# Kernel tuning notes

Measured on AMD Instinct MI355X. Metric: run time of the kernel, lower is better.

## Reference

```python
import jax, jax.numpy as jnp
import numpy as np
import math

S, B, E, H = 2048, 2, 1024, 16
D = E // H
LN_EPS = 1e-5


def setup_inputs() -> dict:
    key = jax.random.key(0)
    ks = jax.random.split(key, 8)
    src = jax.random.normal(ks[0], (S, B, E), dtype=jnp.float32)
    # causal attention mask: 1 = attend, 0 = masked
    src_mask = jnp.tril(jnp.ones((S, S), dtype=jnp.int32))
    in_proj_w = jax.random.normal(ks[1], (2 * E, E), dtype=jnp.float32) * 0.02
    in_proj_b = jnp.zeros((2 * E,), dtype=jnp.float32)
    out_proj_w = jax.random.normal(ks[2], (E, E), dtype=jnp.float32) * 0.02
    out_proj_b = jnp.zeros((E,), dtype=jnp.float32)
    ln_g = jnp.ones((E,), dtype=jnp.float32)
    ln_b = jnp.zeros((E,), dtype=jnp.float32)
    return {"src": src, "src_mask": src_mask, "in_proj_w": in_proj_w,
            "in_proj_b": in_proj_b, "out_proj_w": out_proj_w,
            "out_proj_b": out_proj_b, "ln_g": ln_g, "ln_b": ln_b}


def _layernorm(x, g, b):
    mu = jnp.mean(x, axis=-1, keepdims=True)
    var = jnp.mean(jnp.square(x - mu), axis=-1, keepdims=True)
    return (x - mu) * jax.lax.rsqrt(var + LN_EPS) * g + b


def reference(src, src_mask, in_proj_w, in_proj_b, out_proj_w, out_proj_b, ln_g, ln_b):
    # src: (S, B, E)
    x_norm = _layernorm(src, ln_g, ln_b)
    proj = jax.nn.silu(x_norm @ in_proj_w.T + in_proj_b)     # (S, B, 2E)
    qkv, u = jnp.split(proj, 2, axis=-1)                     # each (S, B, E)
    qkv = qkv.reshape(S, B, H, D)                            # q = k = v = qkv
    # scores: (B, H, S_q, S_k)
    scores = jnp.einsum('sbhd,tbhd->bhst', qkv, qkv) / math.sqrt(D)
    # torch does masked_fill(-inf) then silu; silu(-inf) -> 0 in the limit,
    # which is the intended semantics (masked positions contribute nothing).
    weights = jnp.where(src_mask[None, None, :, :] == 0, 0.0, jax.nn.silu(scores))
    # attn_dropout is identity at eval
    attn = jnp.einsum('bhst,tbhd->sbhd', weights, qkv).reshape(S, B, E)
    gated = attn * u
    out = src + (gated @ out_proj_w.T + out_proj_b)          # out_dropout = identity
    return out
```

## Files before the change

kernel.cpp:

```cpp
#include <hip/hip_runtime.h>


typedef __attribute__((ext_vector_type(8))) short  short8;
typedef __attribute__((ext_vector_type(4))) float  floatx4;
typedef __attribute__((ext_vector_type(4))) float  fvec4;
typedef __attribute__((ext_vector_type(4))) unsigned short usvec4;
typedef __attribute__((ext_vector_type(4))) int    intx4;

__device__ __forceinline__ unsigned short f2b(float f) {
  unsigned u = __builtin_bit_cast(unsigned, f);
  u += 0x7FFFu + ((u >> 16) & 1u);
  return (unsigned short)(u >> 16);
}
__device__ __forceinline__ unsigned short f2b_trunc(float f) {
  return (unsigned short)(__builtin_bit_cast(unsigned, f) >> 16);
}
__device__ __forceinline__ float b2f(unsigned short h) {
  unsigned u = ((unsigned)h) << 16;
  return __builtin_bit_cast(float, u);
}
__device__ __forceinline__ float silu_f(float x) {
  float e = __builtin_amdgcn_exp2f(-1.44269504f * x);
  return x * __builtin_amdgcn_rcpf(1.f + e);
}
__device__ __forceinline__ void async_copy16(void* lds, const void* g) {
  __builtin_amdgcn_global_load_lds(
      (__attribute__((address_space(1))) void*)(g),
      (__attribute__((address_space(3))) void*)(lds), 16, 0, 0);
}

__global__ void cvt_bf16(const float* __restrict__ s1, unsigned short* __restrict__ d1,
                         const float* __restrict__ s2, unsigned short* __restrict__ d2,
                         int n1, int ntot) {
  int i = blockIdx.x * 256 + threadIdx.x;
  if (i >= ntot) return;
  const float* s; unsigned short* d; int j;
  if (i < n1) { s = s1; d = d1; j = i; } else { s = s2; d = d2; j = i - n1; }
  fvec4 v = ((const fvec4*)s)[j];
  usvec4 o = { f2b(v.x), f2b(v.y), f2b(v.z), f2b(v.w) };
  ((usvec4*)d)[j] = o;
}

__global__ __launch_bounds__(256) void ln_kernel(
    const float* __restrict__ x, const float* __restrict__ g,
    const float* __restrict__ b, unsigned short* __restrict__ xn) {
  const int lane = threadIdx.x & 63;
  const int row = blockIdx.x * 4 + (threadIdx.x >> 6);
  const fvec4* xr = (const fvec4*)(x + (long)row * 1024);
  fvec4 v[4];
  float s = 0.f, s2 = 0.f;
  #pragma unroll
  for (int c = 0; c < 4; ++c) {
    v[c] = xr[lane + 64 * c];
    s  += v[c].x + v[c].y + v[c].z + v[c].w;
    s2 += v[c].x*v[c].x + v[c].y*v[c].y + v[c].z*v[c].z + v[c].w*v[c].w;
  }
  #pragma unroll
  for (int off = 32; off; off >>= 1) { s += __shfl_xor(s, off); s2 += __shfl_xor(s2, off); }
  float mu  = s * (1.f / 1024.f);
  float var = s2 * (1.f / 1024.f) - mu * mu;
  float rs  = rsqrtf(var + 1e-5f);
  usvec4* outr = (usvec4*)(xn + (long)row * 1024);
  #pragma unroll
  for (int c = 0; c < 4; ++c) {
    fvec4 gg = ((const fvec4*)g)[lane + 64 * c];
    fvec4 bb = ((const fvec4*)b)[lane + 64 * c];
    usvec4 o = { f2b((v[c].x - mu) * rs * gg.x + bb.x),
                 f2b((v[c].y - mu) * rs * gg.y + bb.y),
                 f2b((v[c].z - mu) * rs * gg.z + bb.z),
                 f2b((v[c].w - mu) * rs * gg.w + bb.w) };
    outr[lane + 64 * c] = o;
  }
}

__global__ __launch_bounds__(256, 2) void gemm_in(
    const unsigned short* __restrict__ A, const unsigned short* __restrict__ Bw,
    const float* __restrict__ bias,
    unsigned short* __restrict__ out0, unsigned short* __restrict__ out1) {
  __shared__ __align__(16) unsigned short sA[128 * 32];
  __shared__ __align__(16) unsigned short sB[128 * 32];
  const int t = threadIdx.x;
  const int lane = t & 63, l15 = lane & 15, quad = lane >> 4;
  const int w = t >> 6, wm = w >> 1, wn = w & 1;
  const int m0 = blockIdx.y * 128, n0 = blockIdx.x * 128;
  const int K = 1024;

  floatx4 acc[4][4];
  const floatx4 z4 = {0.f, 0.f, 0.f, 0.f};
  #pragma unroll
  for (int i = 0; i < 4; i++)
    #pragma unroll
    for (int j = 0; j < 4; j++) acc[i][j] = z4;

  for (int kt = 0; kt < 32; ++kt) {
    const int k0 = kt << 5;
    __syncthreads();
    #pragma unroll
    for (int c = 0; c < 2; ++c) {
      int slot = c * 256 + t;
      int row = slot >> 2, col = (slot & 3) << 3;
      async_copy16(&sA[slot * 8], &A[(m0 + row) * K + k0 + col]);
      async_copy16(&sB[slot * 8], &Bw[(n0 + row) * K + k0 + col]);
    }
    __syncthreads();
    short8 af[4], bf[4];
    #pragma unroll
    for (int mr = 0; mr < 4; mr++)
      af[mr] = *(const short8*)&sA[(wm * 64 + mr * 16 + l15) * 32 + quad * 8];
    #pragma unroll
    for (int nr = 0; nr < 4; nr++)
      bf[nr] = *(const short8*)&sB[(wn * 64 + nr * 16 + l15) * 32 + quad * 8];
    #pragma unroll
    for (int mr = 0; mr < 4; mr++)
      #pragma unroll
      for (int nr = 0; nr < 4; nr++)
        acc[mr][nr] = __builtin_amdgcn_mfma_f32_16x16x32_bf16(af[mr], bf[nr], acc[mr][nr], 0, 0, 0);
  }

  #pragma unroll
  for (int mr = 0; mr < 4; mr++) {
    int gm0 = m0 + wm * 64 + mr * 16 + quad * 4;
    #pragma unroll
    for (int nr = 0; nr < 4; nr++) {
      int gn = n0 + wn * 64 + nr * 16 + l15;
      float bv = bias[gn];
      unsigned short* dst = (gn < 1024) ? (out0 + gn) : (out1 + gn - 1024);
      #pragma unroll
      for (int r = 0; r < 4; r++) {
        float v = acc[mr][nr][r] + bv;
        dst[(long)(gm0 + r) * 1024] = f2b(silu_f(v));
      }
    }
  }
}

__global__ __launch_bounds__(256, 2) void gemm_out(
    const unsigned short* __restrict__ A, const unsigned short* __restrict__ Bw,
    const float* __restrict__ bias, const float* __restrict__ src,
    float* __restrict__ outf) {
  __shared__ __align__(16) unsigned short sA[128 * 32];
  __shared__ __align__(16) unsigned short sB[64 * 32];
  const int t = threadIdx.x;
  const int lane = t & 63, l15 = lane & 15, quad = lane >> 4;
  const int w = t >> 6;
  const int m0 = blockIdx.y * 128, n0 = blockIdx.x * 64;

  floatx4 acc[2][4];
  const floatx4 z4 = {0.f, 0.f, 0.f, 0.f};
  #pragma unroll
  for (int i = 0; i < 2; i++)
    #pragma unroll
    for (int j = 0; j < 4; j++) acc[i][j] = z4;

  for (int kt = 0; kt < 32; ++kt) {
    const int k0 = kt << 5;
    __syncthreads();
    #pragma unroll
    for (int c = 0; c < 2; ++c) {
      int slot = c * 256 + t;
      int row = slot >> 2, col = (slot & 3) << 3;
      async_copy16(&sA[slot * 8], &A[(m0 + row) * 1024 + k0 + col]);
    }
    { int row = t >> 2, col = (t & 3) << 3;
      async_copy16(&sB[t * 8], &Bw[(n0 + row) * 1024 + k0 + col]); }
    __syncthreads();
    short8 af[2], bf[4];
    #pragma unroll
    for (int mr = 0; mr < 2; mr++)
      af[mr] = *(const short8*)&sA[(w * 32 + mr * 16 + l15) * 32 + quad * 8];
    #pragma unroll
    for (int nr = 0; nr < 4; nr++)
      bf[nr] = *(const short8*)&sB[(nr * 16 + l15) * 32 + quad * 8];
    #pragma unroll
    for (int mr = 0; mr < 2; mr++)
      #pragma unroll
      for (int nr = 0; nr < 4; nr++)
        acc[mr][nr] = __builtin_amdgcn_mfma_f32_16x16x32_bf16(af[mr], bf[nr], acc[mr][nr], 0, 0, 0);
  }

  #pragma unroll
  for (int mr = 0; mr < 2; mr++) {
    int gm0 = m0 + w * 32 + mr * 16 + quad * 4;
    #pragma unroll
    for (int nr = 0; nr < 4; nr++) {
      int gn = n0 + nr * 16 + l15;
      float bv = bias[gn];
      #pragma unroll
      for (int r = 0; r < 4; r++) {
        long idx = (long)(gm0 + r) * 1024 + gn;
        outf[idx] = acc[mr][nr][r] + bv + src[idx];
      }
    }
  }
}

#define SKS 72
#define SVS 136
#define SPS 136
#define SOS 68
__global__ __launch_bounds__(256, 2) void attn_kernel(
    const unsigned short* __restrict__ qkv, const unsigned short* __restrict__ u,
    unsigned short* __restrict__ gated) {
  __shared__ __align__(16) unsigned char smem[128 * SKS * 2 + 64 * SVS * 2];
  unsigned short* sK  = (unsigned short*)smem;
  unsigned short* sP  = (unsigned short*)smem;
  unsigned short* sVt = (unsigned short*)(smem + 128 * SKS * 2);
  float*          sO  = (float*)smem;

  const int t = threadIdx.x, lane = t & 63, l15 = lane & 15, quad = lane >> 4;
  const int w = t >> 6;
  const int pair = blockIdx.x >> 5;
  const int bh = blockIdx.x & 31;
  const int b = bh >> 4, h = bh & 15;
  const long base = (long)b * 1024 + h * 64;
  const int rg = t >> 3, dg = t & 7;
  const int swz0 = (rg >> 1) + dg;
  const int d_rd = w * 16 + l15;
  const int rsw0 = quad + (d_rd & 7) + (d_rd >> 3);
  const floatx4 z4 = {0.f, 0.f, 0.f, 0.f};

  for (int half = 0; half < 2; ++half) {
    const int qi = half ? (31 - pair) : pair;
    const int q0 = qi * 64;
    const int nkt = (qi >> 1) + 1;

    if (half) __syncthreads();
    #pragma unroll
    for (int c = 0; c < 2; ++c) {
      int slot = c * 256 + t, row = slot >> 3, cg = slot & 7;
      *(short8*)&sK[row * SKS + cg * 8] =
          *(const short8*)&qkv[base + (long)(q0 + row) * 2048 + cg * 8];
    }
    __syncthreads();
    short8 qf[4][2];
    #pragma unroll
    for (int mr = 0; mr < 4; mr++)
      #pragma unroll
      for (int ks = 0; ks < 2; ks++)
        qf[mr][ks] = *(const short8*)&sK[(mr * 16 + l15) * SKS + ks * 32 + quad * 8];

    floatx4 oacc[4];
    #pragma unroll
    for (int i = 0; i < 4; i++) oacc[i] = z4;

    for (int kt = 0; kt < nkt; ++kt) {
      const int t0 = kt * 128;
      __syncthreads();
      short8 kv[4];
      #pragma unroll
      for (int i = 0; i < 4; ++i)
        kv[i] = *(const short8*)&qkv[base + (long)(t0 + rg * 4 + i) * 2048 + dg * 8];
      #pragma unroll
      for (int i = 0; i < 4; ++i)
        *(short8*)&sK[(rg * 4 + i) * SKS + dg * 8] = kv[i];
      {
        intx4 k0 = __builtin_bit_cast(intx4, kv[0]);
        intx4 k1 = __builtin_bit_cast(intx4, kv[1]);
        intx4 k2 = __builtin_bit_cast(intx4, kv[2]);
        intx4 k3 = __builtin_bit_cast(intx4, kv[3]);
        #pragma unroll
        for (int jj = 0; jj < 4; ++jj) {
          unsigned lo = __builtin_amdgcn_perm((unsigned)k1[jj], (unsigned)k0[jj], 0x05040100u);
          unsigned hi = __builtin_amdgcn_perm((unsigned)k3[jj], (unsigned)k2[jj], 0x05040100u);
          int j = 2 * jj, d = dg * 8 + j;
          int gsw = (swz0 + j) & 15;
          *(unsigned long long*)&sVt[d * SVS + gsw * 8 + (rg & 1) * 4] =
              (unsigned long long)lo | ((unsigned long long)hi << 32);
          lo = __builtin_amdgcn_perm((unsigned)k1[jj], (unsigned)k0[jj], 0x07060302u);
          hi = __builtin_amdgcn_perm((unsigned)k3[jj], (unsigned)k2[jj], 0x07060302u);
          j = 2 * jj + 1; d = dg * 8 + j;
          gsw = (swz0 + j) & 15;
          *(unsigned long long*)&sVt[d * SVS + gsw * 8 + (rg & 1) * 4] =
              (unsigned long long)lo | ((unsigned long long)hi << 32);
        }
      }
      __syncthreads();
      floatx4 sacc[4][2];
      #pragma unroll
      for (int i = 0; i < 4; i++) { sacc[i][0] = z4; sacc[i][1] = z4; }
      #pragma unroll
      for (int ks = 0; ks < 2; ++ks) {
        short8 kf[2];
        #pragma unroll
        for (int nr = 0; nr < 2; nr++)
          kf[nr] = *(const short8*)&sK[(w * 32 + nr * 16 + l15) * SKS + ks * 32 + quad * 8];
        #pragma unroll
        for (int mr = 0; mr < 4; mr++)
          #pragma unroll
          for (int nr = 0; nr < 2; nr++)
            sacc[mr][nr] = __builtin_amdgcn_mfma_f32_16x16x32_bf16(qf[mr][ks], kf[nr], sacc[mr][nr], 0, 0, 0);
      }
      const bool diag = (kt == nkt - 1);
      #pragma unroll
      for (int mr = 0; mr < 4; mr++) {
        int row0 = mr * 16 + quad * 4;
        #pragma unroll
        for (int nr = 0; nr < 2; nr++) {
          int col = w * 32 + nr * 16 + l15;
          #pragma unroll
          for (int r = 0; r < 4; r++) {
            float v = silu_f(sacc[mr][nr][r] * 0.125f);
            if (diag && (q0 + row0 + r < t0 + col)) v = 0.f;
            sacc[mr][nr][r] = v;
          }
        }
      }
      __syncthreads();
      #pragma unroll
      for (int mr = 0; mr < 4; mr++)
        #pragma unroll
        for (int nr = 0; nr < 2; nr++)
          #pragma unroll
          for (int r = 0; r < 4; r++)
            sP[(mr * 16 + quad * 4 + r) * SPS + w * 32 + nr * 16 + l15] =
                f2b_trunc(sacc[mr][nr][r]);
      __syncthreads();
      #pragma unroll
      for (int ts = 0; ts < 4; ++ts) {
        int gsw = (ts * 4 + rsw0) & 15;
        short8 vfr = *(const short8*)&sVt[d_rd * SVS + gsw * 8];
        #pragma unroll
        for (int mr = 0; mr < 4; mr++) {
          short8 pf = *(const short8*)&sP[(mr * 16 + l15) * SPS + ts * 32 + quad * 8];
          oacc[mr] = __builtin_amdgcn_mfma_f32_16x16x32_bf16(pf, vfr, oacc[mr], 0, 0, 0);
        }
      }
    }

    __syncthreads();
    #pragma unroll
    for (int mr = 0; mr < 4; mr++)
      #pragma unroll
      for (int r = 0; r < 4; r++)
        sO[(mr * 16 + quad * 4 + r) * SOS + w * 16 + l15] = oacc[mr][r];
    __syncthreads();
    {
      const int erow = t >> 2, edg = t & 3;
      const float* sOr = sO + erow * SOS + edg * 16;
      const long grow = (long)(q0 + erow) * 2048 + base + edg * 16;
      short8 u0 = *(const short8*)&u[grow];
      short8 u1 = *(const short8*)&u[grow + 8];
      short8 g0, g1;
      #pragma unroll
      for (int j = 0; j < 8; ++j) {
        g0[j] = (short)f2b(sOr[j]     * b2f((unsigned short)u0[j]));
        g1[j] = (short)f2b(sOr[j + 8] * b2f((unsigned short)u1[j]));
      }
      *(short8*)&gated[grow]     = g0;
      *(short8*)&gated[grow + 8] = g1;
    }
  }
}

extern "C" void kernel_launch(void* const* d_in, const int* in_sizes, int n_in,
                              void* d_out, int out_size, void* d_ws, size_t ws_size,
                              hipStream_t stream) {
  const float* src = (const float*)d_in[0];
  const float* w1  = (const float*)d_in[2];
  const float* b1  = (const float*)d_in[3];
  const float* w2  = (const float*)d_in[4];
  const float* b2  = (const float*)d_in[5];
  const float* lng = (const float*)d_in[6];
  const float* lnb = (const float*)d_in[7];
  float* out = (float*)d_out;

  char* ws = (char*)d_ws;
  unsigned short* xn    = (unsigned short*)(ws + 0);
  unsigned short* qkv   = (unsigned short*)(ws + 8388608);
  unsigned short* uu    = (unsigned short*)(ws + 16777216);
  unsigned short* gated = (unsigned short*)(ws + 25165824);
  unsigned short* w1b   = (unsigned short*)(ws + 33554432);
  unsigned short* w2b   = (unsigned short*)(ws + 37748736);

  cvt_bf16<<<3072, 256, 0, stream>>>(w1, w1b, w2, w2b, 524288, 786432);
  ln_kernel<<<1024, 256, 0, stream>>>(src, lng, lnb, xn);
  gemm_in<<<dim3(16, 32), 256, 0, stream>>>(xn, w1b, b1, qkv, uu);
  attn_kernel<<<512, 256, 0, stream>>>(qkv, uu, gated);
  gemm_out<<<dim3(16, 32), 256, 0, stream>>>(gated, w2b, b2, src, out);
}
```

Before: 190.7 us.

## Restructure attention: register-resident P via bpermute, double-buffered V, split-K reduction

Computes S transposed (K as the A operand, Q as B), so each wave owns 32 key rows for all 64 queries. P is converted to bf16 in registers and shuffled into MFMA operand layout with ds_bpermute, which removes the LDS round-trip for P and two barriers per tile. V^T is double-buffered and the next K/V tile is loaded into registers early so global latency overlaps compute. Each wave now holds partial O over its key slice, so a cross-wave reduction through LDS is added at the end, and the oacc[4][4] accumulators raise register pressure.

```diff
diff --git a/kernel.cpp b/kernel.cpp
--- a/kernel.cpp
+++ b/kernel.cpp
@@ -11,9 +11,6 @@
   unsigned u = __builtin_bit_cast(unsigned, f);
   u += 0x7FFFu + ((u >> 16) & 1u);
   return (unsigned short)(u >> 16);
-}
-__device__ __forceinline__ unsigned short f2b_trunc(float f) {
-  return (unsigned short)(__builtin_bit_cast(unsigned, f) >> 16);
 }
 __device__ __forceinline__ float b2f(unsigned short h) {
   unsigned u = ((unsigned)h) << 16;
@@ -196,27 +193,53 @@
 
 #define SKS 72
 #define SVS 136
-#define SPS 136
-#define SOS 68
+__device__ __forceinline__ void write_kv(unsigned short* sKp, unsigned short* sVp,
+                                         const short8* kv, int rg, int dg, int swz0) {
+  #pragma unroll
+  for (int i = 0; i < 4; ++i)
+    *(short8*)&sKp[(rg * 4 + i) * SKS + dg * 8] = kv[i];
+  intx4 k0 = __builtin_bit_cast(intx4, kv[0]);
+  intx4 k1 = __builtin_bit_cast(intx4, kv[1]);
+  intx4 k2 = __builtin_bit_cast(intx4, kv[2]);
+  intx4 k3 = __builtin_bit_cast(intx4, kv[3]);
+  #pragma unroll
+  for (int jj = 0; jj < 4; ++jj) {
+    unsigned lo = __builtin_amdgcn_perm((unsigned)k1[jj], (unsigned)k0[jj], 0x05040100u);
+    unsigned hi = __builtin_amdgcn_perm((unsigned)k3[jj], (unsigned)k2[jj], 0x05040100u);
+    int j = 2 * jj, d = dg * 8 + j;
+    int gsw = (swz0 + j) & 15;
+    *(unsigned long long*)&sVp[d * SVS + gsw * 8 + (rg & 1) * 4] =
+        (unsigned long long)lo | ((unsigned long long)hi << 32);
+    lo = __builtin_amdgcn_perm((unsigned)k1[jj], (unsigned)k0[jj], 0x07060302u);
+    hi = __builtin_amdgcn_perm((unsigned)k3[jj], (unsigned)k2[jj], 0x07060302u);
+    j = 2 * jj + 1; d = dg * 8 + j;
+    gsw = (swz0 + j) & 15;
+    *(unsigned long long*)&sVp[d * SVS + gsw * 8 + (rg & 1) * 4] =
+        (unsigned long long)lo | ((unsigned long long)hi << 32);
+  }
+}
+
 __global__ __launch_bounds__(256, 2) void attn_kernel(
     const unsigned short* __restrict__ qkv, const unsigned short* __restrict__ u,
     unsigned short* __restrict__ gated) {
-  __shared__ __align__(16) unsigned char smem[128 * SKS * 2 + 64 * SVS * 2];
-  unsigned short* sK  = (unsigned short*)smem;
-  unsigned short* sP  = (unsigned short*)smem;
-  unsigned short* sVt = (unsigned short*)(smem + 128 * SKS * 2);
-  float*          sO  = (float*)smem;
+  __shared__ __align__(16) unsigned char smem[18432 + 2 * 17408];
+  unsigned short* sK   = (unsigned short*)smem;
+  unsigned short* sVt0 = (unsigned short*)(smem + 18432);
+  unsigned short* sVt1 = (unsigned short*)(smem + 18432 + 17408);
+  unsigned short* sQ   = sVt1;
+  float*          sR   = (float*)smem;
 
   const int t = threadIdx.x, lane = t & 63, l15 = lane & 15, quad = lane >> 4;
   const int w = t >> 6;
-  const int pair = blockIdx.x >> 5;
-  const int bh = blockIdx.x & 31;
+  const int pair = blockIdx.x >> 5, bh = blockIdx.x & 31;
   const int b = bh >> 4, h = bh & 15;
   const long base = (long)b * 1024 + h * 64;
   const int rg = t >> 3, dg = t & 7;
   const int swz0 = (rg >> 1) + dg;
-  const int d_rd = w * 16 + l15;
-  const int rsw0 = quad + (d_rd & 7) + (d_rd >> 3);
+  const int addr_lo = 4 * (l15 + 32 * (quad & 1));
+  const int addr_hi = addr_lo + 64;
+  const bool qhi = quad >= 2;
+  const int vswz = w * 4 + quad + (l15 & 7) + (l15 >> 3);
   const floatx4 z4 = {0.f, 0.f, 0.f, 0.f};
 
   for (int half = 0; half < 2; ++half) {
@@ -228,123 +251,154 @@
     #pragma unroll
     for (int c = 0; c < 2; ++c) {
       int slot = c * 256 + t, row = slot >> 3, cg = slot & 7;
-      *(short8*)&sK[row * SKS + cg * 8] =
+      *(short8*)&sQ[row * SKS + cg * 8] =
           *(const short8*)&qkv[base + (long)(q0 + row) * 2048 + cg * 8];
     }
     __syncthreads();
     short8 qf[4][2];
     #pragma unroll
-    for (int mr = 0; mr < 4; mr++)
+    for (int nt = 0; nt < 4; nt++)
       #pragma unroll
       for (int ks = 0; ks < 2; ks++)
-        qf[mr][ks] = *(const short8*)&sK[(mr * 16 + l15) * SKS + ks * 32 + quad * 8];
-
-    floatx4 oacc[4];
-    #pragma unroll
-    for (int i = 0; i < 4; i++) oacc[i] = z4;
+        qf[nt][ks] = *(const short8*)&sQ[(nt * 16 + l15) * SKS + ks * 32 + quad * 8];
+    short8 kv[4];
+    #pragma unroll
+    for (int i = 0; i < 4; ++i)
+      kv[i] = *(const short8*)&qkv[base + (long)(rg * 4 + i) * 2048 + dg * 8];
+    write_kv(sK, sVt0, kv, rg, dg, swz0);
+
+    floatx4 oacc[4][4];
+    #pragma unroll
+    for (int i = 0; i < 4; i++)
+      #pragma unroll
+      for (int j = 0; j < 4; j++) oacc[i][j] = z4;
 
     for (int kt = 0; kt < nkt; ++kt) {
-      const int t0 = kt * 128;
+      unsigned short* sVtC = (kt & 1) ? sVt1 : sVt0;
+      unsigned short* sVtN = (kt & 1) ? sVt0 : sVt1;
       __syncthreads();
-      short8 kv[4];
-      #pragma unroll
-      for (int i = 0; i < 4; ++i)
-        kv[i] = *(const short8*)&qkv[base + (long)(t0 + rg * 4 + i) * 2048 + dg * 8];
-      #pragma unroll
-      for (int i = 0; i < 4; ++i)
-        *(short8*)&sK[(rg * 4 + i) * SKS + dg * 8] = kv[i];
-      {
-        intx4 k0 = __builtin_bit_cast(intx4, kv[0]);
-        intx4 k1 = __builtin_bit_cast(intx4, kv[1]);
-        intx4 k2 = __builtin_bit_cast(intx4, kv[2]);
-        intx4 k3 = __builtin_bit_cast(intx4, kv[3]);
-        #pragma unroll
-        for (int jj = 0; jj < 4; ++jj) {
-          unsigned lo = __builtin_amdgcn_perm((unsigned)k1[jj], (unsigned)k0[jj], 0x05040100u);
-          unsigned hi = __builtin_amdgcn_perm((unsigned)k3[jj], (unsigned)k2[jj], 0x05040100u);
-          int j = 2 * jj, d = dg * 8 + j;
-          int gsw = (swz0 + j) & 15;
-          *(unsigned long long*)&sVt[d * SVS + gsw * 8 + (rg & 1) * 4] =
-              (unsigned long long)lo | ((unsigned long long)hi << 32);
-          lo = __builtin_amdgcn_perm((unsigned)k1[jj], (unsigned)k0[jj], 0x07060302u);
-          hi = __builtin_amdgcn_perm((unsigned)k3[jj], (unsigned)k2[jj], 0x07060302u);
-          j = 2 * jj + 1; d = dg * 8 + j;
-          gsw = (swz0 + j) & 15;
-          *(unsigned long long*)&sVt[d * SVS + gsw * 8 + (rg & 1) * 4] =
-              (unsigned long long)lo | ((unsigned long long)hi << 32);
+      const bool more = (kt + 1 < nkt);
+      if (more) {
+        const long nb = base + (long)((kt + 1) * 128) * 2048;
+        #pragma unroll
+        for (int i = 0; i < 4; ++i)
+          kv[i] = *(const short8*)&qkv[nb + (long)(rg * 4 + i) * 2048 + dg * 8];
+      }
+      short8 kf[2][2];
+      #pragma unroll
+      for (int mt = 0; mt < 2; mt++)
+        #pragma unroll
+        for (int ks = 0; ks < 2; ks++)
+          kf[mt][ks] = *(const short8*)&sK[(w * 32 + mt * 16 + l15) * SKS + ks * 32 + quad * 8];
+      __syncthreads();
+      floatx4 sacc[2][4];
+      #pragma unroll
+      for (int i = 0; i < 2; i++)
+        #pragma unroll
+        for (int j = 0; j < 4; j++) sacc[i][j] = z4;
+      #pragma unroll
+      for (int ks = 0; ks < 2; ++ks)
+        #pragma unroll
+        for (int mt = 0; mt < 2; mt++)
+          #pragma unroll
+          for (int nt = 0; nt < 4; nt++)
+            sacc[mt][nt] = __builtin_amdgcn_mfma_f32_16x16x32_bf16(
+                kf[mt][ks], qf[nt][ks], sacc[mt][nt], 0, 0, 0);
+      const bool diag = (kt == nkt - 1);
+      const int tw = kt * 128 + w * 32;
+      unsigned p0[2][4], p1[2][4];
+      #pragma unroll
+      for (int mt = 0; mt < 2; mt++)
+        #pragma unroll
+        for (int nt = 0; nt < 4; nt++) {
+          float v[4];
+          if (diag) {
+            int qq = q0 + nt * 16 + l15;
+            #pragma unroll
+            for (int r = 0; r < 4; r++) {
+              int tt = tw + mt * 16 + quad * 4 + r;
+              float x = silu_f(sacc[mt][nt][r] * 0.125f);
+              v[r] = (qq < tt) ? 0.f : x;
+            }
+          } else {
+            #pragma unroll
+            for (int r = 0; r < 4; r++) v[r] = silu_f(sacc[mt][nt][r] * 0.125f);
+          }
+          p0[mt][nt] = __builtin_amdgcn_perm(__builtin_bit_cast(unsigned, v[1]),
+                                             __builtin_bit_cast(unsigned, v[0]), 0x07060302u);
+          p1[mt][nt] = __builtin_amdgcn_perm(__builtin_bit_cast(unsigned, v[3]),
+                                             __builtin_bit_cast(unsigned, v[2]), 0x07060302u);
         }
-      }
-      __syncthreads();
-      floatx4 sacc[4][2];
-      #pragma unroll
-      for (int i = 0; i < 4; i++) { sacc[i][0] = z4; sacc[i][1] = z4; }
-      #pragma unroll
-      for (int ks = 0; ks < 2; ++ks) {
-        short8 kf[2];
-        #pragma unroll
-        for (int nr = 0; nr < 2; nr++)
-          kf[nr] = *(const short8*)&sK[(w * 32 + nr * 16 + l15) * SKS + ks * 32 + quad * 8];
-        #pragma unroll
-        for (int mr = 0; mr < 4; mr++)
-          #pragma unroll
-          for (int nr = 0; nr < 2; nr++)
-            sacc[mr][nr] = __builtin_amdgcn_mfma_f32_16x16x32_bf16(qf[mr][ks], kf[nr], sacc[mr][nr], 0, 0, 0);
-      }
-      const bool diag = (kt == nkt - 1);
-      #pragma unroll
-      for (int mr = 0; mr < 4; mr++) {
-        int row0 = mr * 16 + quad * 4;
-        #pragma unroll
-        for (int nr = 0; nr < 2; nr++) {
-          int col = w * 32 + nr * 16 + l15;
-          #pragma unroll
-          for (int r = 0; r < 4; r++) {
-            float v = silu_f(sacc[mr][nr][r] * 0.125f);
-            if (diag && (q0 + row0 + r < t0 + col)) v = 0.f;
-            sacc[mr][nr][r] = v;
+      short8 vb[4];
+      #pragma unroll
+      for (int dt = 0; dt < 4; dt++)
+        vb[dt] = *(const short8*)&sVtC[(dt * 16 + l15) * SVS + ((vswz + 2 * dt) & 15) * 8];
+      #pragma unroll
+      for (int qt = 0; qt < 4; qt++) {
+        intx4 pa;
+        #pragma unroll
+        for (int jj = 0; jj < 4; jj++) {
+          int addr = (jj >> 1) ? addr_hi : addr_lo;
+          int lo, hi;
+          if (jj & 1) {
+            lo = __builtin_amdgcn_ds_bpermute(addr, (int)p1[0][qt]);
+            hi = __builtin_amdgcn_ds_bpermute(addr, (int)p1[1][qt]);
+          } else {
+            lo = __builtin_amdgcn_ds_bpermute(addr, (int)p0[0][qt]);
+            hi = __builtin_amdgcn_ds_bpermute(addr, (int)p0[1][qt]);
           }
+          pa[jj] = qhi ? hi : lo;
         }
-      }
-      __syncthreads();
-      #pragma unroll
-      for (int mr = 0; mr < 4; mr++)
-        #pragma unroll
-        for (int nr = 0; nr < 2; nr++)
+        short8 paf = __builtin_bit_cast(short8, pa);
+        #pragma unroll
+        for (int dt = 0; dt < 4; dt++)
+          oacc[qt][dt] = __builtin_amdgcn_mfma_f32_16x16x32_bf16(paf, vb[dt], oacc[qt][dt], 0, 0, 0);
+      }
+      if (more) write_kv(sK, sVtN, kv, rg, dg, swz0);
+    }
+
+    __syncthreads();
+    float* plane = sR + (w & 1) * 4352;
+    if (w < 2) {
+      #pragma unroll
+      for (int qt = 0; qt < 4; qt++)
+        #pragma unroll
+        for (int dt = 0; dt < 4; dt++)
           #pragma unroll
           for (int r = 0; r < 4; r++)
-            sP[(mr * 16 + quad * 4 + r) * SPS + w * 32 + nr * 16 + l15] =
-                f2b_trunc(sacc[mr][nr][r]);
-      __syncthreads();
-      #pragma unroll
-      for (int ts = 0; ts < 4; ++ts) {
-        int gsw = (ts * 4 + rsw0) & 15;
-        short8 vfr = *(const short8*)&sVt[d_rd * SVS + gsw * 8];
-        #pragma unroll
-        for (int mr = 0; mr < 4; mr++) {
-          short8 pf = *(const short8*)&sP[(mr * 16 + l15) * SPS + ts * 32 + quad * 8];
-          oacc[mr] = __builtin_amdgcn_mfma_f32_16x16x32_bf16(pf, vfr, oacc[mr], 0, 0, 0);
-        }
-      }
-    }
-
-    __syncthreads();
-    #pragma unroll
-    for (int mr = 0; mr < 4; mr++)
-      #pragma unroll
-      for (int r = 0; r < 4; r++)
-        sO[(mr * 16 + quad * 4 + r) * SOS + w * 16 + l15] = oacc[mr][r];
+            plane[(qt * 16 + quad * 4 + r) * 68 + dt * 16 + l15] = oacc[qt][dt][r];
+    }
+    __syncthreads();
+    if (w >= 2) {
+      #pragma unroll
+      for (int qt = 0; qt < 4; qt++)
+        #pragma unroll
+        for (int dt = 0; dt < 4; dt++)
+          #pragma unroll
+          for (int r = 0; r < 4; r++)
+            plane[(qt * 16 + quad * 4 + r) * 68 + dt * 16 + l15] += oacc[qt][dt][r];
+    }
     __syncthreads();
     {
       const int erow = t >> 2, edg = t & 3;
-      const float* sOr = sO + erow * SOS + edg * 16;
       const long grow = (long)(q0 + erow) * 2048 + base + edg * 16;
       short8 u0 = *(const short8*)&u[grow];
       short8 u1 = *(const short8*)&u[grow + 8];
+      const float* r0p = sR + erow * 68 + edg * 16;
+      const float* r1p = r0p + 4352;
+      float o[16];
+      #pragma unroll
+      for (int c = 0; c < 4; c++) {
+        fvec4 a = ((const fvec4*)r0p)[c];
+        fvec4 bsum = ((const fvec4*)r1p)[c];
+        o[4*c+0] = a.x + bsum.x; o[4*c+1] = a.y + bsum.y;
+        o[4*c+2] = a.z + bsum.z; o[4*c+3] = a.w + bsum.w;
+      }
       short8 g0, g1;
       #pragma unroll
       for (int j = 0; j < 8; ++j) {
-        g0[j] = (short)f2b(sOr[j]     * b2f((unsigned short)u0[j]));
-        g1[j] = (short)f2b(sOr[j + 8] * b2f((unsigned short)u1[j]));
+        g0[j] = (short)f2b(o[j]     * b2f((unsigned short)u0[j]));
+        g1[j] = (short)f2b(o[j + 8] * b2f((unsigned short)u1[j]));
       }
       *(short8*)&gated[grow]     = g0;
       *(short8*)&gated[grow + 8] = g1;
```

Result: no change. 190.9 us (+0.2%).
